# Optimization experiments

Hardware: AMD Instinct MI355X
Metric: run time of the kernel (lower is better)

The kernel has to match this reference:

```python
import jax, jax.numpy as jnp
import numpy as np
from jax import lax

WINDOW = 40          # plan.window_size
E = 8                # len(plan.expand_feature)
F = 64               # len(plan.feature)
OUT_CH = 128
KERNEL = 5
ALPHA = 0.01         # leaky_relu_alpha
N_LABEL = 1


def time_conv(x, conv_size):
    """x: [N, T, F] -> [N, WINDOW, 5*E] sliding-window stats over first E features."""
    N, T, _ = x.shape
    begin = T - (conv_size + WINDOW - 1)
    xe = x[:, :, :E]                                             # [N, T, E]
    idx = begin + jnp.arange(WINDOW)[:, None] + jnp.arange(conv_size)[None, :]  # [W, C]
    win = xe[:, idx, :]                                          # [N, W, C, E]
    _mean = win.mean(axis=2)                                     # [N, W, E]
    _std = jnp.std(win, axis=2, ddof=1)                          # torch.std is unbiased
    _max = win.max(axis=2)
    _min = win.min(axis=2)
    # rank of last timestep of each window, cross-sectionally over stocks (dim 0)
    last = xe[:, begin + conv_size - 1: begin + conv_size - 1 + WINDOW, :]  # [N, W, E]
    order = jnp.argsort(-last, axis=0)
    rank = jnp.argsort(order, axis=0).astype(x.dtype) / N        # [N, W, E]
    return jnp.concatenate([_mean, _std, rank, _max, _min], axis=2)  # [N, W, 5E]


def setup_inputs() -> dict:
    key = jax.random.key(0)
    k1, k2, k3, k4, k5 = jax.random.split(key, 5)
    N, T = 8000, 64
    in_ch = F + 10 * E  # 144
    x = jax.random.normal(k1, (N, T, F), dtype=jnp.float32)
    conv_w = jax.random.normal(k2, (OUT_CH, in_ch, KERNEL), dtype=jnp.float32) * 0.05
    conv_b = jax.random.normal(k3, (OUT_CH,), dtype=jnp.float32) * 0.05
    lin_in = WINDOW + 1 - KERNEL  # 36
    lin_w = jax.random.normal(k4, (N_LABEL, lin_in), dtype=jnp.float32) * 0.1
    lin_b = jax.random.normal(k5, (N_LABEL,), dtype=jnp.float32) * 0.1
    return {"x": x, "conv_w": conv_w, "conv_b": conv_b, "lin_w": lin_w, "lin_b": lin_b}


def reference(x, conv_w, conv_b, lin_w, lin_b):
    week_x = time_conv(x, conv_size=5)     # [N, W, 5E]
    month_x = time_conv(x, conv_size=20)   # [N, W, 5E]
    xc = jnp.concatenate([x[:, -WINDOW:, :], week_x, month_x], axis=2)  # [N, W, F+10E]
    cnn_x = jnp.transpose(xc, (0, 2, 1))   # [N, C, W]
    part = lax.conv_general_dilated(cnn_x, conv_w, window_strides=(1,),
                                    padding='VALID',
                                    dimension_numbers=('NCH', 'OIH', 'NCH'))
    part = part + conv_b[None, :, None]    # [N, OUT_CH, W+1-K]
    h = part[:, -1, :]                     # last output channel, [N, W+1-K]
    h = jnp.where(h >= 0, h, ALPHA * h)    # leaky relu
    return h @ lin_w.T + lin_b             # [N, N_LABEL]
```

## Files before the change

### kernel.cpp

```cpp
#include <hip/hip_runtime.h>
#include <math.h>

#define NS    8000
#define TT    64
#define FF    64
#define EE    8
#define WIN   40
#define TR    59
#define NBINS 1024

#define XET_SZ  (8*59*8000)
#define RNK_SZ  (8*40*8000)

__global__ __launch_bounds__(256) void k_transpose(const float* __restrict__ x,
                                                   float* __restrict__ xeT) {
    int n = blockIdx.x * 256 + threadIdx.x;
    int r = blockIdx.y;
    if (n >= NS) return;
    const float* row = x + (size_t)n * (TT * FF) + (5 + r) * FF;
    float4 a = *(const float4*)(row);
    float4 b = *(const float4*)(row + 4);
    xeT[(0 * TR + r) * NS + n] = a.x;
    xeT[(1 * TR + r) * NS + n] = a.y;
    xeT[(2 * TR + r) * NS + n] = a.z;
    xeT[(3 * TR + r) * NS + n] = a.w;
    xeT[(4 * TR + r) * NS + n] = b.x;
    xeT[(5 * TR + r) * NS + n] = b.y;
    xeT[(6 * TR + r) * NS + n] = b.z;
    xeT[(7 * TR + r) * NS + n] = b.w;
}

__device__ __forceinline__ int binOf(float v) {
    int b = (int)((v + 4.0f) * 128.0f);
    b = b < 0 ? 0 : b;
    return b > (NBINS - 1) ? (NBINS - 1) : b;
}

__global__ __launch_bounds__(1024) void k_rank(const float* __restrict__ xeT,
                                               float* __restrict__ rankT) {
    const int w = blockIdx.x;
    const int e = blockIdx.y;
    __shared__ unsigned hist[NBINS];
    __shared__ unsigned basev[NBINS];
    __shared__ unsigned bendv[NBINS];
    __shared__ float          sk[NS];
    __shared__ unsigned short si[NS];
    __shared__ unsigned wsum[16];

    const int tid  = threadIdx.x;
    const int lane = tid & 63;
    const int wid  = tid >> 6;
    const float* col = xeT + ((size_t)e * TR + (19 + w)) * NS;

    float val[8];
#pragma unroll
    for (int i = 0; i < 8; i++) {
        int idx = tid + i * 1024;
        val[i] = (idx < NS) ? col[idx] : 0.0f;
    }
    hist[tid] = 0;
    __syncthreads();

#pragma unroll
    for (int i = 0; i < 8; i++) {
        int idx = tid + i * 1024;
        if (idx < NS) atomicAdd(&hist[binOf(val[i])], 1u);
    }
    __syncthreads();

    unsigned h = hist[tid];
    unsigned sc = h;
#pragma unroll
    for (int d = 1; d < 64; d <<= 1) {
        unsigned t2 = __shfl_up(sc, d);
        if (lane >= d) sc += t2;
    }
    if (lane == 63) wsum[wid] = sc;
    __syncthreads();
    unsigned woff = 0;
    for (int i = 0; i < wid; i++) woff += wsum[i];
    unsigned before = woff + (sc - h);
    bendv[tid] = NS - before;
    basev[tid] = NS - before - h;
    hist[tid]  = NS - before - h;
    __syncthreads();

#pragma unroll
    for (int i = 0; i < 8; i++) {
        int idx = tid + i * 1024;
        if (idx < NS) {
            int b = binOf(val[i]);
            unsigned p = atomicAdd(&hist[b], 1u);
            sk[p] = val[i];
            si[p] = (unsigned short)idx;
        }
    }
    __syncthreads();

    float* outp = rankT + ((size_t)e * WIN + w) * NS;
#pragma unroll 1
    for (int i = 0; i < 8; i++) {
        int p = tid + i * 1024;
        if (p < NS) {
            float v = sk[p];
            unsigned idm = si[p];
            int b = binOf(v);
            unsigned lo = basev[b], hi = bendv[b];
            unsigned c = 0;
            for (unsigned q = lo; q < hi; q++) {
                float u2 = sk[q];
                c += (u2 > v) || (u2 == v && si[q] < idm);
            }
            outp[idm] = (float)(basev[b] + c) / 8000.0f;
        }
    }
}

__global__ __launch_bounds__(128) void k_stats(const float* __restrict__ x,
                                               const float* __restrict__ cw,
                                               const float* __restrict__ xeT,
                                               const float* __restrict__ rankT,
                                               float* __restrict__ uT) {
    const int n  = blockIdx.x * 128 + threadIdx.x;
    const int w0 = blockIdx.y * 4;
    if (n >= NS) return;
    const float* W = cw + 127 * 144 * 5;

    float g[4][5];
#pragma unroll
    for (int dw = 0; dw < 4; dw++)
#pragma unroll
        for (int k = 0; k < 5; k++) g[dw][k] = 0.0f;

    {
        const float* row = x + (size_t)n * (TT * FF) + (24 + w0) * FF;
#pragma unroll
        for (int dw = 0; dw < 4; dw++) {
            const float* r2 = row + dw * FF;
#pragma unroll
            for (int f = 0; f < FF; f += 4) {
                float4 a = *(const float4*)(r2 + f);
#pragma unroll
                for (int k = 0; k < 5; k++) {
                    g[dw][k] += a.x * W[(f + 0) * 5 + k] + a.y * W[(f + 1) * 5 + k]
                              + a.z * W[(f + 2) * 5 + k] + a.w * W[(f + 3) * 5 + k];
                }
            }
        }
    }

    for (int e = 0; e < 8; e++) {
        const float* colbase = xeT + ((size_t)e * TR + w0) * NS + n;
        float xv[23];
#pragma unroll
        for (int j = 0; j < 23; j++) xv[j] = colbase[(size_t)j * NS];

#pragma unroll
        for (int dw = 0; dw < 4; dw++) {
            float s20 = 0.f, mn20 = xv[dw], mx20 = xv[dw];
#pragma unroll
            for (int i = 0; i < 20; i++) {
                float v = xv[dw + i];
                s20 += v; mn20 = fminf(mn20, v); mx20 = fmaxf(mx20, v);
            }
            float m20 = s20 * (1.0f / 20.0f);
            float d20 = 0.f;
#pragma unroll
            for (int i = 0; i < 20; i++) { float t = xv[dw + i] - m20; d20 += t * t; }
            float sd20 = sqrtf(d20 * (1.0f / 19.0f));

            float s5 = 0.f, mn5 = xv[dw + 15], mx5 = xv[dw + 15];
#pragma unroll
            for (int i = 15; i < 20; i++) {
                float v = xv[dw + i];
                s5 += v; mn5 = fminf(mn5, v); mx5 = fmaxf(mx5, v);
            }
            float m5 = s5 * 0.2f;
            float d5 = 0.f;
#pragma unroll
            for (int i = 15; i < 20; i++) { float t = xv[dw + i] - m5; d5 += t * t; }
            float sd5 = sqrtf(d5 * 0.25f);

            float rk = rankT[((size_t)e * WIN + (w0 + dw)) * NS + n];

#pragma unroll
            for (int k = 0; k < 5; k++) {
                float uk;
                uk  = m5   * W[(64  + e) * 5 + k];
                uk += sd5  * W[(72  + e) * 5 + k];
                uk += rk   * (W[(80 + e) * 5 + k] + W[(120 + e) * 5 + k]);
                uk += mx5  * W[(88  + e) * 5 + k];
                uk += mn5  * W[(96  + e) * 5 + k];
                uk += m20  * W[(104 + e) * 5 + k];
                uk += sd20 * W[(112 + e) * 5 + k];
                uk += mx20 * W[(128 + e) * 5 + k];
                uk += mn20 * W[(136 + e) * 5 + k];
                g[dw][k] += uk;
            }
        }
    }

#pragma unroll
    for (int dw = 0; dw < 4; dw++)
#pragma unroll
        for (int k = 0; k < 5; k++)
            uT[(size_t)((w0 + dw) * 5 + k) * NS + n] = g[dw][k];
}

__global__ __launch_bounds__(256) void k_final(const float* __restrict__ uT,
                                               const float* __restrict__ cb,
                                               const float* __restrict__ lw,
                                               const float* __restrict__ lb,
                                               float* __restrict__ outp) {
    int n = blockIdx.x * 256 + threadIdx.x;
    if (n >= NS) return;
    float b127 = cb[127];
    float acc = lb[0];
#pragma unroll
    for (int j = 0; j < 36; j++) {
        float g = b127;
#pragma unroll
        for (int k = 0; k < 5; k++) {
            g += uT[(size_t)((j + k) * 5 + k) * NS + n];
        }
        g = (g >= 0.0f) ? g : 0.01f * g;
        acc += g * lw[j];
    }
    outp[n] = acc;
}

extern "C" void kernel_launch(void* const* d_in, const int* in_sizes, int n_in,
                              void* d_out, int out_size, void* d_ws, size_t ws_size,
                              hipStream_t stream) {
    const float* x  = (const float*)d_in[0];
    const float* cw = (const float*)d_in[1];
    const float* cb = (const float*)d_in[2];
    const float* lw = (const float*)d_in[3];
    const float* lb = (const float*)d_in[4];
    float* outp = (float*)d_out;

    float* ws    = (float*)d_ws;
    float* xeT   = ws;
    float* rankT = ws + XET_SZ;
    float* uT    = ws + XET_SZ + RNK_SZ;

    k_transpose<<<dim3(32, 59), 256, 0, stream>>>(x, xeT);
    k_rank<<<dim3(WIN, EE), 1024, 0, stream>>>(xeT, rankT);
    k_stats<<<dim3(63, 10), 128, 0, stream>>>(x, cw, xeT, rankT, uT);
    k_final<<<32, 256, 0, stream>>>(uT, cb, lw, lb, outp);
}
```

Measured before the change: 276.7 us.

## Split stats kernel into coalesced raw-feature projection and per-window derived-stat kernels

The fused k_stats kernel is split in two. k_raw projects the raw 64 features with a 16-lane-per-row layout, using coalesced float4 loads and a shuffle reduction, with the weights kept in registers. k_derived computes the derived stats with one window per thread instead of four, which raises parallelism. The intent is to replace strided per-thread loads of whole x rows with coalesced loads and to improve occupancy. In exchange it adds a kernel launch, an extra workspace buffer, re-reads of overlapping xeT windows, and strided per-n reads of uraw in k_final.

```diff
diff --git a/kernel.cpp b/kernel.cpp
--- a/kernel.cpp
+++ b/kernel.cpp
@@ -11,6 +11,7 @@
 
 #define XET_SZ  (8*59*8000)
 #define RNK_SZ  (8*40*8000)
+#define UDER_SZ (40*5*8000)
 
 __global__ __launch_bounds__(256) void k_transpose(const float* __restrict__ x,
                                                    float* __restrict__ xeT) {
@@ -116,98 +117,121 @@
     }
 }
 
-__global__ __launch_bounds__(128) void k_stats(const float* __restrict__ x,
-                                               const float* __restrict__ cw,
-                                               const float* __restrict__ xeT,
-                                               const float* __restrict__ rankT,
-                                               float* __restrict__ uT) {
-    const int n  = blockIdx.x * 128 + threadIdx.x;
-    const int w0 = blockIdx.y * 4;
+__global__ __launch_bounds__(256) void k_raw(const float* __restrict__ x,
+                                             const float* __restrict__ cw,
+                                             float* __restrict__ uraw) {
+    const int n    = blockIdx.x * 4 + (threadIdx.x >> 6);
+    const int lane = threadIdx.x & 63;
+    const int g    = lane >> 4;
+    const int l    = lane & 15;
+    const float* W = cw + 127 * 144 * 5;
+
+    float wreg[20];
+    {
+        const float4* Wq = (const float4*)(W + l * 20);
+#pragma unroll
+        for (int q = 0; q < 5; q++) {
+            float4 t = Wq[q];
+            wreg[q * 4 + 0] = t.x; wreg[q * 4 + 1] = t.y;
+            wreg[q * 4 + 2] = t.z; wreg[q * 4 + 3] = t.w;
+        }
+    }
+
+    const float* xbase = x + (size_t)n * (TT * FF) + 24 * FF + l * 4;
+    float* ubase = uraw + (size_t)n * (WIN * 5);
+
+#pragma unroll 1
+    for (int w0 = 0; w0 < WIN; w0 += 4) {
+        const int w = w0 + g;
+        float4 xv = *(const float4*)(xbase + w * FF);
+        float acc[5];
+#pragma unroll
+        for (int k = 0; k < 5; k++) {
+            acc[k] = xv.x * wreg[0 * 5 + k] + xv.y * wreg[1 * 5 + k]
+                   + xv.z * wreg[2 * 5 + k] + xv.w * wreg[3 * 5 + k];
+        }
+#pragma unroll
+        for (int d = 1; d < 16; d <<= 1) {
+#pragma unroll
+            for (int k = 0; k < 5; k++) acc[k] += __shfl_xor(acc[k], d, 64);
+        }
+        if (l < 5) {
+            float v = acc[0];
+            if (l == 1) v = acc[1];
+            else if (l == 2) v = acc[2];
+            else if (l == 3) v = acc[3];
+            else if (l == 4) v = acc[4];
+            ubase[w * 5 + l] = v;
+        }
+    }
+}
+
+__global__ __launch_bounds__(256) void k_der(const float* __restrict__ cw,
+                                             const float* __restrict__ xeT,
+                                             const float* __restrict__ rankT,
+                                             float* __restrict__ uder) {
+    const int n = blockIdx.x * 256 + threadIdx.x;
+    const int w = blockIdx.y;
     if (n >= NS) return;
     const float* W = cw + 127 * 144 * 5;
 
-    float g[4][5];
-#pragma unroll
-    for (int dw = 0; dw < 4; dw++)
-#pragma unroll
-        for (int k = 0; k < 5; k++) g[dw][k] = 0.0f;
-
-    {
-        const float* row = x + (size_t)n * (TT * FF) + (24 + w0) * FF;
-#pragma unroll
-        for (int dw = 0; dw < 4; dw++) {
-            const float* r2 = row + dw * FF;
-#pragma unroll
-            for (int f = 0; f < FF; f += 4) {
-                float4 a = *(const float4*)(r2 + f);
-#pragma unroll
-                for (int k = 0; k < 5; k++) {
-                    g[dw][k] += a.x * W[(f + 0) * 5 + k] + a.y * W[(f + 1) * 5 + k]
-                              + a.z * W[(f + 2) * 5 + k] + a.w * W[(f + 3) * 5 + k];
-                }
-            }
-        }
-    }
+    float g[5] = {0.f, 0.f, 0.f, 0.f, 0.f};
 
     for (int e = 0; e < 8; e++) {
-        const float* colbase = xeT + ((size_t)e * TR + w0) * NS + n;
-        float xv[23];
-#pragma unroll
-        for (int j = 0; j < 23; j++) xv[j] = colbase[(size_t)j * NS];
-
-#pragma unroll
-        for (int dw = 0; dw < 4; dw++) {
-            float s20 = 0.f, mn20 = xv[dw], mx20 = xv[dw];
-#pragma unroll
-            for (int i = 0; i < 20; i++) {
-                float v = xv[dw + i];
-                s20 += v; mn20 = fminf(mn20, v); mx20 = fmaxf(mx20, v);
-            }
-            float m20 = s20 * (1.0f / 20.0f);
-            float d20 = 0.f;
-#pragma unroll
-            for (int i = 0; i < 20; i++) { float t = xv[dw + i] - m20; d20 += t * t; }
-            float sd20 = sqrtf(d20 * (1.0f / 19.0f));
-
-            float s5 = 0.f, mn5 = xv[dw + 15], mx5 = xv[dw + 15];
-#pragma unroll
-            for (int i = 15; i < 20; i++) {
-                float v = xv[dw + i];
-                s5 += v; mn5 = fminf(mn5, v); mx5 = fmaxf(mx5, v);
-            }
-            float m5 = s5 * 0.2f;
-            float d5 = 0.f;
-#pragma unroll
-            for (int i = 15; i < 20; i++) { float t = xv[dw + i] - m5; d5 += t * t; }
-            float sd5 = sqrtf(d5 * 0.25f);
-
-            float rk = rankT[((size_t)e * WIN + (w0 + dw)) * NS + n];
-
-#pragma unroll
-            for (int k = 0; k < 5; k++) {
-                float uk;
-                uk  = m5   * W[(64  + e) * 5 + k];
-                uk += sd5  * W[(72  + e) * 5 + k];
-                uk += rk   * (W[(80 + e) * 5 + k] + W[(120 + e) * 5 + k]);
-                uk += mx5  * W[(88  + e) * 5 + k];
-                uk += mn5  * W[(96  + e) * 5 + k];
-                uk += m20  * W[(104 + e) * 5 + k];
-                uk += sd20 * W[(112 + e) * 5 + k];
-                uk += mx20 * W[(128 + e) * 5 + k];
-                uk += mn20 * W[(136 + e) * 5 + k];
-                g[dw][k] += uk;
-            }
-        }
-    }
-
-#pragma unroll
-    for (int dw = 0; dw < 4; dw++)
-#pragma unroll
-        for (int k = 0; k < 5; k++)
-            uT[(size_t)((w0 + dw) * 5 + k) * NS + n] = g[dw][k];
-}
-
-__global__ __launch_bounds__(256) void k_final(const float* __restrict__ uT,
+        const float* colbase = xeT + ((size_t)e * TR + w) * NS + n;
+        float xv[20];
+#pragma unroll
+        for (int j = 0; j < 20; j++) xv[j] = colbase[(size_t)j * NS];
+
+        float s20 = 0.f, mn20 = xv[0], mx20 = xv[0];
+#pragma unroll
+        for (int i = 0; i < 20; i++) {
+            float v = xv[i];
+            s20 += v; mn20 = fminf(mn20, v); mx20 = fmaxf(mx20, v);
+        }
+        float m20 = s20 * (1.0f / 20.0f);
+        float d20 = 0.f;
+#pragma unroll
+        for (int i = 0; i < 20; i++) { float t = xv[i] - m20; d20 += t * t; }
+        float sd20 = sqrtf(d20 * (1.0f / 19.0f));
+
+        float s5 = 0.f, mn5 = xv[15], mx5 = xv[15];
+#pragma unroll
+        for (int i = 15; i < 20; i++) {
+            float v = xv[i];
+            s5 += v; mn5 = fminf(mn5, v); mx5 = fmaxf(mx5, v);
+        }
+        float m5 = s5 * 0.2f;
+        float d5 = 0.f;
+#pragma unroll
+        for (int i = 15; i < 20; i++) { float t = xv[i] - m5; d5 += t * t; }
+        float sd5 = sqrtf(d5 * 0.25f);
+
+        float rk = rankT[((size_t)e * WIN + w) * NS + n];
+
+#pragma unroll
+        for (int k = 0; k < 5; k++) {
+            float uk;
+            uk  = m5   * W[(64  + e) * 5 + k];
+            uk += sd5  * W[(72  + e) * 5 + k];
+            uk += rk   * (W[(80 + e) * 5 + k] + W[(120 + e) * 5 + k]);
+            uk += mx5  * W[(88  + e) * 5 + k];
+            uk += mn5  * W[(96  + e) * 5 + k];
+            uk += m20  * W[(104 + e) * 5 + k];
+            uk += sd20 * W[(112 + e) * 5 + k];
+            uk += mx20 * W[(128 + e) * 5 + k];
+            uk += mn20 * W[(136 + e) * 5 + k];
+            g[k] += uk;
+        }
+    }
+
+#pragma unroll
+    for (int k = 0; k < 5; k++)
+        uder[(size_t)(w * 5 + k) * NS + n] = g[k];
+}
+
+__global__ __launch_bounds__(256) void k_final(const float* __restrict__ uraw,
+                                               const float* __restrict__ uder,
                                                const float* __restrict__ cb,
                                                const float* __restrict__ lw,
                                                const float* __restrict__ lb,
@@ -216,12 +240,14 @@
     if (n >= NS) return;
     float b127 = cb[127];
     float acc = lb[0];
+    const float* ur = uraw + (size_t)n * (WIN * 5);
 #pragma unroll
     for (int j = 0; j < 36; j++) {
         float g = b127;
 #pragma unroll
         for (int k = 0; k < 5; k++) {
-            g += uT[(size_t)((j + k) * 5 + k) * NS + n];
+            int c = (j + k) * 5 + k;
+            g += ur[c] + uder[(size_t)c * NS + n];
         }
         g = (g >= 0.0f) ? g : 0.01f * g;
         acc += g * lw[j];
@@ -242,10 +268,12 @@
     float* ws    = (float*)d_ws;
     float* xeT   = ws;
     float* rankT = ws + XET_SZ;
-    float* uT    = ws + XET_SZ + RNK_SZ;
+    float* uder  = ws + XET_SZ + RNK_SZ;
+    float* uraw  = ws + XET_SZ + RNK_SZ + UDER_SZ;
 
     k_transpose<<<dim3(32, 59), 256, 0, stream>>>(x, xeT);
     k_rank<<<dim3(WIN, EE), 1024, 0, stream>>>(xeT, rankT);
-    k_stats<<<dim3(63, 10), 128, 0, stream>>>(x, cw, xeT, rankT, uT);
-    k_final<<<32, 256, 0, stream>>>(uT, cb, lw, lb, outp);
-}
+    k_raw<<<2000, 256, 0, stream>>>(x, cw, uraw);
+    k_der<<<dim3(32, WIN), 256, 0, stream>>>(cw, xeT, rankT, uder);
+    k_final<<<32, 256, 0, stream>>>(uraw, uder, cb, lw, lb, outp);
+}
```

Result: faster. 269.6 us (-2.6%).
